# Performance work log

Hardware: AMD Instinct MI355X
Metric: run time of the kernel (lower is better)

## Reference

```python
import jax, jax.numpy as jnp
import numpy as np
from collections import deque

N, IN_DIM, H, B, L = 512, 64, 128, 256, 2
SOURCE = 105
E_UND = 2048


def _build_graph_and_masks():
    rng = np.random.default_rng(0)
    s = rng.integers(0, N, E_UND)
    d = rng.integers(0, N, E_UND)
    edge_index = np.stack([np.concatenate([s, d]), np.concatenate([d, s])]).astype(np.int32)
    # BFS depths from source (undirected)
    adj = [[] for _ in range(N)]
    for a, b in zip(edge_index[0], edge_index[1]):
        adj[int(a)].append(int(b))
    depths = np.full(N, np.inf)
    depths[SOURCE] = 0.0
    q = deque([SOURCE]); seen = {SOURCE}
    while q:
        u = q.popleft()
        for v in adj[u]:
            if v not in seen:
                seen.add(v); depths[v] = depths[u] + 1.0; q.append(v)
    finite = np.isfinite(depths)
    maxd = depths[finite].max() if finite.any() else 0.0
    depths[~finite] = maxd + 1.0
    adj_mask = np.zeros((N, N), np.float32)
    adj_mask[edge_index[0], edge_index[1]] = 1.0
    adj_mask[edge_index[1], edge_index[0]] = 1.0
    np.fill_diagonal(adj_mask, 1.0)
    direction_mask = (depths[None, :] <= depths[:, None]).astype(np.float32)
    # admittance_matrix is None -> uniform init, then masked
    initial_causal = (np.ones((N, N), np.float32) / N) * adj_mask * direction_mask
    return edge_index, adj_mask, direction_mask, initial_causal


def setup_inputs() -> dict:
    key = jax.random.key(0)
    ks = jax.random.split(key, 16)
    edge_index, adj_mask, direction_mask, initial_causal = _build_graph_and_masks()
    w = lambda k, shp: jax.random.normal(k, shp, jnp.float32) * 0.02
    return {
        'x': jax.random.normal(ks[0], (B, N, IN_DIM), jnp.float32),
        'edge_index': jnp.asarray(edge_index),
        'adj_mask': jnp.asarray(adj_mask),
        'direction_mask': jnp.asarray(direction_mask),
        'causal_logits': jnp.asarray(initial_causal),  # nn.Parameter init
        'W_in': w(ks[1], (IN_DIM, H)), 'b_in': jnp.zeros((H,), jnp.float32),
        'Wq': w(ks[2], (H, H)), 'bq': jnp.zeros((H,), jnp.float32),
        'Wk': w(ks[3], (H, H)), 'bk': jnp.zeros((H,), jnp.float32),
        'Wv': w(ks[4], (H, H)), 'bv': jnp.zeros((H,), jnp.float32),
        'gcn_W': w(ks[5], (L, H, H)), 'gcn_b': jnp.zeros((L, H), jnp.float32),
        'W_fuse': w(ks[6], (2 * H, H)), 'b_fuse': jnp.zeros((H,), jnp.float32),
        'ln_g': jnp.ones((H,), jnp.float32), 'ln_b': jnp.zeros((H,), jnp.float32),
    }


def reference(x, edge_index, adj_mask, direction_mask, causal_logits,
              W_in, b_in, Wq, bq, Wk, bk, Wv, bv,
              gcn_W, gcn_b, W_fuse, b_fuse, ln_g, ln_b):
    n = adj_mask.shape[0]
    h = jax.nn.relu(x @ W_in + b_in)                               # (B,N,H)

    # causal matrix: softmax over learned logits, physically masked, renormalized
    C = jax.nn.softmax(causal_logits, axis=-1) * adj_mask * direction_mask
    C = C / jnp.clip(C.sum(-1, keepdims=True), 1e-8)

    # masked causal attention
    Q = h @ Wq + bq; K = h @ Wk + bk; V = h @ Wv + bv
    scale = jnp.asarray(h.shape[-1] ** 0.5, h.dtype)
    attn = jax.nn.softmax(jnp.einsum('bnh,bmh->bnm', Q, K) / scale, axis=-1)
    attn = attn * C[None]
    attn = attn / (attn.sum(-1, keepdims=True) + 1e-8)
    h_causal = jnp.einsum('bnm,bmh->bnh', attn, V)

    # GCNConv stack (self-loops + symmetric norm; dropout is identity in eval)
    src = jnp.concatenate([edge_index[0], jnp.arange(n, dtype=edge_index.dtype)])
    dst = jnp.concatenate([edge_index[1], jnp.arange(n, dtype=edge_index.dtype)])
    deg = jnp.zeros((n,), h.dtype).at[dst].add(1.0)
    dinv = deg ** -0.5                                              # deg>=1 (self loops)
    norm = (dinv[src] * dinv[dst])[None, :, None]                   # (1,E+N,1)
    h_g = h
    for l in range(gcn_W.shape[0]):
        hW = h_g @ gcn_W[l]                                         # (B,N,H)
        msg = hW[:, src, :] * norm                                  # (B,E+N,H)
        h_g = jnp.zeros_like(hW).at[:, dst, :].add(msg) + gcn_b[l]
        h_g = jax.nn.relu(h_g)

    h_comb = jnp.concatenate([h_causal, h_g], axis=-1) @ W_fuse + b_fuse
    mu = h_comb.mean(-1, keepdims=True)
    var = ((h_comb - mu) ** 2).mean(-1, keepdims=True)
    out = (h_comb - mu) / jnp.sqrt(var + 1e-5) * ln_g + ln_b
    return out, C
```

## Files before the change

### kernel.cpp

```cpp
#include <hip/hip_runtime.h>
#include <hip/hip_bf16.h>
#include <math.h>

#define NN 512
#define HH 128
#define INDIM 64
#define BB 256
#define NE 4096
#define MROWS (BB*NN)
#define OUT0 (BB*NN*HH)

typedef __attribute__((ext_vector_type(8))) short short8v;
typedef __attribute__((ext_vector_type(4))) float float4v;

__device__ __forceinline__ unsigned short f2bf(float f) {
  unsigned u = __float_as_uint(f);
  unsigned r = (u + 0x7fffu + ((u >> 16) & 1u)) >> 16;
  return (unsigned short)r;
}
__device__ __forceinline__ float bf2f(unsigned short b) {
  return __uint_as_float(((unsigned)b) << 16);
}

__global__ __launch_bounds__(256) void k_causalC(
    const float* __restrict__ logits, const float* __restrict__ adj,
    const float* __restrict__ dir, float* __restrict__ Cout)
{
  const int row = blockIdx.x;
  const int t = threadIdx.x;
  __shared__ float red[256];
  const float* lrow = logits + (size_t)row * NN;
  float v0 = lrow[t], v1 = lrow[t + 256];
  float mx = fmaxf(v0, v1);
  red[t] = mx; __syncthreads();
  for (int s = 128; s > 0; s >>= 1) { if (t < s) red[t] = fmaxf(red[t], red[t + s]); __syncthreads(); }
  mx = red[0]; __syncthreads();
  float e0 = __expf(v0 - mx), e1 = __expf(v1 - mx);
  red[t] = e0 + e1; __syncthreads();
  for (int s = 128; s > 0; s >>= 1) { if (t < s) red[t] += red[t + s]; __syncthreads(); }
  float sumE = red[0]; __syncthreads();
  float m0 = adj[(size_t)row * NN + t] * dir[(size_t)row * NN + t];
  float m1 = adj[(size_t)row * NN + t + 256] * dir[(size_t)row * NN + t + 256];
  float me0 = e0 * m0, me1 = e1 * m1;
  red[t] = me0 + me1; __syncthreads();
  for (int s = 128; s > 0; s >>= 1) { if (t < s) red[t] += red[t + s]; __syncthreads(); }
  float sumME = red[0];
  float sm = sumME / sumE;
  float denom = fmaxf(sm, 1e-8f) * sumE;
  Cout[(size_t)row * NN + t]       = me0 / denom;
  Cout[(size_t)row * NN + t + 256] = me1 / denom;
}

__global__ __launch_bounds__(512) void k_csr(const int* __restrict__ ei,
                                             int* __restrict__ rp,
                                             int* __restrict__ ci,
                                             float* __restrict__ cw)
{
  __shared__ int scnt[512];
  __shared__ float sdinv[512];
  __shared__ int sval[512];
  __shared__ int scur[512];
  const int t = threadIdx.x;
  const int* src = ei;
  const int* dst = ei + NE;
  scnt[t] = 0;
  __syncthreads();
  for (int e = t; e < NE; e += 512) atomicAdd(&scnt[dst[e]], 1);
  __syncthreads();
  const int deg = scnt[t] + 1;
  sdinv[t] = rsqrtf((float)deg);
  sval[t] = deg;
  __syncthreads();
  for (int off = 1; off < 512; off <<= 1) {
    int add = (t >= off) ? sval[t - off] : 0;
    __syncthreads();
    sval[t] += add;
    __syncthreads();
  }
  const int excl = sval[t] - deg;
  rp[t] = excl;
  if (t == 511) rp[512] = excl + deg;
  ci[excl] = t;
  cw[excl] = sdinv[t] * sdinv[t];
  scur[t] = excl + 1;
  __syncthreads();
  for (int e = t; e < NE; e += 512) {
    int s = src[e], d = dst[e];
    int p = atomicAdd(&scur[d], 1);
    ci[p] = s;
    cw[p] = sdinv[s] * sdinv[d];
  }
}

__global__ __launch_bounds__(512) void k_ccsr(const int* __restrict__ ei,
                                              const float* __restrict__ Cmat,
                                              int* __restrict__ rp,
                                              int* __restrict__ ci,
                                              float* __restrict__ cw)
{
  __shared__ unsigned bm[512 * 16];
  __shared__ int cnt[512];
  __shared__ int sval[512];
  __shared__ int cur[512];
  const int t = threadIdx.x;
  const int* src = ei;
  const int* dst = ei + NE;
  for (int i = t; i < 512 * 16; i += 512) bm[i] = 0u;
  __syncthreads();
  bm[t * 16 + (t >> 5)] |= (1u << (t & 31));
  cnt[t] = 1;
  __syncthreads();
  for (int e = t; e < NE; e += 512) {
    int r = src[e], c = dst[e];
    if (Cmat[(size_t)r * NN + c] > 0.f) {
      unsigned bit = 1u << (c & 31);
      unsigned old = atomicOr(&bm[r * 16 + (c >> 5)], bit);
      if (!(old & bit)) atomicAdd(&cnt[r], 1);
    }
  }
  __syncthreads();
  const int myc = cnt[t];
  sval[t] = myc;
  __syncthreads();
  for (int off = 1; off < 512; off <<= 1) {
    int add = (t >= off) ? sval[t - off] : 0;
    __syncthreads();
    sval[t] += add;
    __syncthreads();
  }
  const int excl = sval[t] - myc;
  rp[t] = excl;
  if (t == 511) rp[512] = excl + myc;
  ci[excl] = t;
  cw[excl] = Cmat[(size_t)t * NN + t];
  cur[t] = excl + 1;
  bm[t * 16 + (t >> 5)] &= ~(1u << (t & 31));
  __syncthreads();
  for (int e = t; e < NE; e += 512) {
    int r = src[e], c = dst[e];
    if (Cmat[(size_t)r * NN + c] > 0.f) {
      unsigned bit = 1u << (c & 31);
      unsigned old = atomicAnd(&bm[r * 16 + (c >> 5)], ~bit);
      if (old & bit) {
        int p = atomicAdd(&cur[r], 1);
        ci[p] = c;
        cw[p] = Cmat[(size_t)r * NN + c];
      }
    }
  }
}

__device__ __forceinline__ void gcn_body(
    int bid, const unsigned short* __restrict__ hW,
    const int* __restrict__ rp, const int* __restrict__ ci,
    const float* __restrict__ cw, const float* __restrict__ bias,
    unsigned short* __restrict__ out, int OS, int OC0)
{
  const int i5 = bid >> 3;
  const int ng = i5 & 31;
  const int b = (bid & 7) * 32 + (i5 >> 5);
  const int t = threadIdx.x;
  const int node = ng * 16 + (t >> 4);
  const int f0 = (t & 15) * 8;

  float bcol[8];
  #pragma unroll
  for (int k = 0; k < 8; k++) bcol[k] = bias[f0 + k];

  const unsigned short* base = hW + (size_t)b * 512 * 128;
  const int beg = rp[node], end = rp[node + 1];
  float acc[8] = {0.f, 0.f, 0.f, 0.f, 0.f, 0.f, 0.f, 0.f};
  for (int j = beg; j < end; j++) {
    int s = ci[j];
    float w = cw[j];
    short8v v = *(const short8v*)&base[(size_t)s * 128 + f0];
    #pragma unroll
    for (int k = 0; k < 8; k++) acc[k] += w * bf2f((unsigned short)v[k]);
  }
  short8v o;
  #pragma unroll
  for (int k = 0; k < 8; k++) {
    float v = fmaxf(acc[k] + bcol[k], 0.f);
    o[k] = (short)f2bf(v);
  }
  *(short8v*)&out[((size_t)(b * 512 + node)) * OS + OC0 + f0] = o;
}

__global__ __launch_bounds__(256) void k_gcn(
    const unsigned short* __restrict__ hW,
    const int* __restrict__ rp, const int* __restrict__ ci,
    const float* __restrict__ cw, const float* __restrict__ bias,
    unsigned short* __restrict__ out, int OS, int OC0)
{
  gcn_body(blockIdx.x, hW, rp, ci, cw, bias, out, OS, OC0);
}

__device__ __forceinline__ void sattn_body(
    int bid, const unsigned short* __restrict__ Qbf,
    const unsigned short* __restrict__ Kbf, const unsigned short* __restrict__ Vbf,
    const int* __restrict__ rp, const int* __restrict__ ci,
    const float* __restrict__ cw, unsigned short* __restrict__ Ocb)
{
  const int i5 = bid >> 3;
  const int ng = i5 & 31;
  const int b = (bid & 7) * 32 + (i5 >> 5);
  const int t = threadIdx.x;
  const int node = ng * 16 + (t >> 4);
  const int f0 = (t & 15) * 8;
  const float scale = 0.088388347648318447f;

  const size_t rowq = ((size_t)(b * 512 + node)) * 128 + f0;
  short8v qv = *(const short8v*)&Qbf[rowq];
  float qf[8];
  #pragma unroll
  for (int k = 0; k < 8; k++) qf[k] = bf2f((unsigned short)qv[k]);

  const unsigned short* Kb = Kbf + (size_t)b * 512 * 128;
  const unsigned short* Vb = Vbf + (size_t)b * 512 * 128;
  const int beg = rp[node], end = rp[node + 1];
  float acc[8] = {0.f, 0.f, 0.f, 0.f, 0.f, 0.f, 0.f, 0.f};
  float sw = 0.f;
  int j = beg;
  float w0 = cw[j];
  int m = ci[j];
  short8v kv = *(const short8v*)&Kb[(size_t)m * 128 + f0];
  short8v vv = *(const short8v*)&Vb[(size_t)m * 128 + f0];
  for (; j < end; ) {
    const int jn = (j + 1 < end) ? j + 1 : j;
    const float w02 = cw[jn];
    const int m2 = ci[jn];
    short8v kv2 = *(const short8v*)&Kb[(size_t)m2 * 128 + f0];
    short8v vv2 = *(const short8v*)&Vb[(size_t)m2 * 128 + f0];
    float part = 0.f;
    #pragma unroll
    for (int k = 0; k < 8; k++) part += qf[k] * bf2f((unsigned short)kv[k]);
    part += __shfl_xor(part, 1);
    part += __shfl_xor(part, 2);
    part += __shfl_xor(part, 4);
    part += __shfl_xor(part, 8);
    float w = __expf(part * scale) * w0;
    sw += w;
    #pragma unroll
    for (int k = 0; k < 8; k++) acc[k] += w * bf2f((unsigned short)vv[k]);
    j++;
    w0 = w02; kv = kv2; vv = vv2;
  }
  float inv = 1.0f / sw;
  short8v o;
  #pragma unroll
  for (int k = 0; k < 8; k++) o[k] = (short)f2bf(acc[k] * inv);
  *(short8v*)&Ocb[((size_t)(b * 512 + node)) * 256 + f0] = o;
}

__global__ __launch_bounds__(256) void k_gs(
    const unsigned short* __restrict__ hW,
    const int* __restrict__ grp, const int* __restrict__ gci,
    const float* __restrict__ gcw, const float* __restrict__ gbias,
    const unsigned short* __restrict__ Qbf, const unsigned short* __restrict__ Kbf,
    const unsigned short* __restrict__ Vbf,
    const int* __restrict__ arp, const int* __restrict__ aci,
    const float* __restrict__ acw,
    unsigned short* __restrict__ Dout)
{
  if (blockIdx.x < 8192)
    gcn_body(blockIdx.x, hW, grp, gci, gcw, gbias, Dout, 256, 128);
  else
    sattn_body(blockIdx.x - 8192, Qbf, Kbf, Vbf, arp, aci, acw, Dout);
}

__global__ __launch_bounds__(256) void k_wt(
    const float* s0, const float* s1, const float* s2, const float* s3,
    const float* s4, const float* s5, const float* s6,
    unsigned short* d0, unsigned short* d1, unsigned short* d2, unsigned short* d3,
    unsigned short* d4, unsigned short* d5, unsigned short* d6)
{
  const float* srcs[7] = {s0, s1, s2, s3, s4, s5, s6};
  unsigned short* dsts[7] = {d0, d1, d2, d3, d4, d5, d6};
  const int Ks[7] = {64, 128, 128, 128, 128, 128, 256};
  const int j = blockIdx.x >> 3;
  const int nc = blockIdx.x & 7;
  const float* s = srcs[j];
  unsigned short* d = dsts[j];
  const int K = Ks[j];
  const int STRW = K + 8;
  const int n0 = nc * 16;
  __shared__ short tile[16 * 264];
  const int t = threadIdx.x;
  for (int i = t; i < K * 16; i += 256) {
    int k = i >> 4, nn = i & 15;
    tile[nn * STRW + k] = (short)f2bf(s[k * 128 + n0 + nn]);
  }
  __syncthreads();
  for (int i = t; i < K * 2; i += 256) {
    int nn = (i * 8) / K;
    int k  = (i * 8) % K;
    *(short8v*)&d[(size_t)(n0 + nn) * K + k] =
        *(const short8v*)&tile[nn * STRW + k];
  }
}

#define GNT 4
template<int KD, bool RELU, bool BATCHW, int OMODE, bool AF32>
__global__ __launch_bounds__(256) void k_bgemm(
    const void* __restrict__ Ap, const unsigned short* __restrict__ Wt,
    const float* __restrict__ bias, void* __restrict__ Out, int OS,
    const float* __restrict__ lng, const float* __restrict__ lnb)
{
  constexpr int KCH = (KD < 128) ? KD : 128;
  constexpr int STR = KCH + 8;
  constexpr bool WONCE = (KD <= 128);
  constexpr int ASH = (64 * STR > 8192) ? 64 * STR : 8192;
  constexpr int TRIPS = KCH / 32;
  __shared__ short lds[ASH + 128 * STR];
  short* As = lds;
  short* Ws = lds + ASH;
  const unsigned short* Abf = (const unsigned short*)Ap;
  const float* Af = (const float*)Ap;
  const int t = threadIdx.x;
  const int wave = t >> 6, lane = t & 63;
  const int l15 = lane & 15, quad = lane >> 4;

  short8v ap[TRIPS];
  float4 fa[TRIPS], fb[TRIPS];

  auto LOADC = [&](int rb, int kc) {
    #pragma unroll
    for (int j = 0; j < TRIPS; j++) {
      int i = t + j * 256;
      int r = i / (KCH / 8), seg = i % (KCH / 8);
      if (AF32) {
        const float* sp = &Af[(size_t)(rb + r) * KD + kc + seg * 8];
        fa[j] = *(const float4*)sp;
        fb[j] = *(const float4*)(sp + 4);
      } else {
        int arow = BATCHW ? ((rb & 511) + r) : (rb + r);
        ap[j] = *(const short8v*)&Abf[(size_t)arow * KD + kc + seg * 8];
      }
    }
  };
  auto STOREC = [&]() {
    #pragma unroll
    for (int j = 0; j < TRIPS; j++) {
      int i = t + j * 256;
      int r = i / (KCH / 8), seg = i % (KCH / 8);
      if (AF32) {
        short8v pk;
        pk[0] = (short)f2bf(fa[j].x); pk[1] = (short)f2bf(fa[j].y);
        pk[2] = (short)f2bf(fa[j].z); pk[3] = (short)f2bf(fa[j].w);
        pk[4] = (short)f2bf(fb[j].x); pk[5] = (short)f2bf(fb[j].y);
        pk[6] = (short)f2bf(fb[j].z); pk[7] = (short)f2bf(fb[j].w);
        *(short8v*)&As[r * STR + seg * 8] = pk;
      } else {
        *(short8v*)&As[r * STR + seg * 8] = ap[j];
      }
    }
  };

  float bcol[8];
  #pragma unroll
  for (int nt = 0; nt < 8; nt++) bcol[nt] = bias ? bias[nt * 16 + l15] : 0.f;
  float gcol[8], bbcol[8];
  if (OMODE == 2) {
    #pragma unroll
    for (int nt = 0; nt < 8; nt++) { gcol[nt] = lng[nt * 16 + l15]; bbcol[nt] = lnb[nt * 16 + l15]; }
  }

  for (int g = blockIdx.x; g < (MROWS / 64) / GNT; g += gridDim.x) {
    if (WONCE) {
      const int b0 = (g * GNT * 64) >> 9;
      const unsigned short* Wb = BATCHW ? (Wt + (size_t)b0 * 128 * KD) : Wt;
      for (int i = t; i < 128 * (KCH / 8); i += 256) {
        int n = i / (KCH / 8), seg = i % (KCH / 8);
        *(short8v*)&Ws[n * STR + seg * 8] =
            *(const short8v*)&Wb[(size_t)n * KD + seg * 8];
      }
    }
    LOADC(g * GNT * 64, 0);
    for (int tt = 0; tt < GNT; tt++) {
      const int tile = g * GNT + tt;
      const int rowbase = tile * 64;
      const int b = rowbase >> 9;
      float4v acc[8];
      #pragma unroll
      for (int nt = 0; nt < 8; nt++) acc[nt] = (float4v){0.f, 0.f, 0.f, 0.f};

      for (int kc = 0; kc < KD; kc += KCH) {
        __syncthreads();
        STOREC();
        if (!WONCE) {
          const unsigned short* Wb = BATCHW ? (Wt + (size_t)b * 128 * KD) : Wt;
          for (int i = t; i < 128 * (KCH / 8); i += 256) {
            int n = i / (KCH / 8), seg = i % (KCH / 8);
            *(short8v*)&Ws[n * STR + seg * 8] =
                *(const short8v*)&Wb[(size_t)n * KD + kc + seg * 8];
          }
        }
        __syncthreads();
        {
          int nkc = kc + KCH, ntt = tt;
          if (nkc >= KD) { nkc = 0; ntt = tt + 1; }
          if (ntt < GNT) LOADC((g * GNT + ntt) * 64, nkc);
        }
        #pragma unroll
        for (int k32 = 0; k32 < KCH / 32; k32++) {
          short8v af = *(const short8v*)&As[(wave * 16 + l15) * STR + k32 * 32 + quad * 8];
          #pragma unroll
          for (int nt = 0; nt < 8; nt++) {
            short8v wf = *(const short8v*)&Ws[(nt * 16 + l15) * STR + k32 * 32 + quad * 8];
            acc[nt] = __builtin_amdgcn_mfma_f32_16x16x32_bf16(af, wf, acc[nt], 0, 0, 0);
          }
        }
      }

      __syncthreads();
      if (OMODE == 0) {
        short* rep = As + wave * 2048;
        #pragma unroll
        for (int nt = 0; nt < 8; nt++)
          #pragma unroll
          for (int r = 0; r < 4; r++) {
            float v = acc[nt][r] + bcol[nt];
            if (RELU) v = fmaxf(v, 0.f);
            rep[(quad * 4 + r) * 128 + nt * 16 + l15] = (short)f2bf(v);
          }
        __syncthreads();
        unsigned short* Ob = (unsigned short*)Out;
        #pragma unroll
        for (int p = 0; p < 4; p++) {
          int row16 = (lane >> 4) + p * 4, seg = lane & 15;
          short8v vv = *(const short8v*)&rep[row16 * 128 + seg * 8];
          *(short8v*)&Ob[(size_t)(rowbase + wave * 16 + row16) * OS + seg * 8] = vv;
        }
      } else if (OMODE == 1) {
        short* rep = As + wave * 2048;
        #pragma unroll
        for (int nt = 0; nt < 8; nt++)
          #pragma unroll
          for (int r = 0; r < 4; r++) {
            float v = acc[nt][r] + bcol[nt];
            if (RELU) v = fmaxf(v, 0.f);
            rep[(nt * 16 + l15) * 16 + quad * 4 + r] = (short)f2bf(v);
          }
        __syncthreads();
        unsigned short* Ob = (unsigned short*)Out;
        int node0 = (rowbase & 511) + wave * 16;
        #pragma unroll
        for (int p = 0; p < 4; p++) {
          int idx = p * 64 + lane, c = idx >> 1, half = idx & 1;
          short8v vv = *(const short8v*)&rep[c * 16 + half * 8];
          *(short8v*)&Ob[((size_t)(b * 128 + c)) * 512 + node0 + half * 8] = vv;
        }
      } else {
        float* repw = (float*)lds + wave * 2048;
        float vv[8][4];
        float s[4] = {0, 0, 0, 0}, ss[4] = {0, 0, 0, 0};
        #pragma unroll
        for (int nt = 0; nt < 8; nt++)
          #pragma unroll
          for (int r = 0; r < 4; r++) {
            float v = acc[nt][r] + bcol[nt];
            vv[nt][r] = v;
            s[r] += v; ss[r] += v * v;
          }
        #pragma unroll
        for (int r = 0; r < 4; r++) {
          s[r] += __shfl_xor(s[r], 1);  s[r] += __shfl_xor(s[r], 2);
          s[r] += __shfl_xor(s[r], 4);  s[r] += __shfl_xor(s[r], 8);
          ss[r] += __shfl_xor(ss[r], 1); ss[r] += __shfl_xor(ss[r], 2);
          ss[r] += __shfl_xor(ss[r], 4); ss[r] += __shfl_xor(ss[r], 8);
        }
        #pragma unroll
        for (int r = 0; r < 4; r++) {
          float mu = s[r] * (1.0f / 128.0f);
          float var = ss[r] * (1.0f / 128.0f) - mu * mu;
          float inv = rsqrtf(var + 1e-5f);
          #pragma unroll
          for (int nt = 0; nt < 8; nt++)
            repw[(quad * 4 + r) * 128 + nt * 16 + l15] =
                (vv[nt][r] - mu) * inv * gcol[nt] + bbcol[nt];
        }
        __syncthreads();
        float* Of = (float*)Out;
        #pragma unroll
        for (int p = 0; p < 8; p++) {
          int row16 = (lane >> 5) + p * 2, seg = lane & 31;
          float4 o = *(const float4*)&repw[row16 * 128 + seg * 4];
          *(float4*)&Of[(size_t)(rowbase + wave * 16 + row16) * 128 + seg * 4] = o;
        }
      }
    }
  }
}

__global__ __launch_bounds__(256) void k_qkv4(
    const unsigned short* __restrict__ Abf,
    const unsigned short* __restrict__ W0, const unsigned short* __restrict__ W1,
    const unsigned short* __restrict__ W2, const unsigned short* __restrict__ W3,
    const float* __restrict__ b1, const float* __restrict__ b2,
    const float* __restrict__ b3,
    unsigned short* __restrict__ O0, unsigned short* __restrict__ O1,
    unsigned short* __restrict__ O2, unsigned short* __restrict__ O3)
{
  constexpr int STR = 136;
  __shared__ short lds[8704 + 128 * STR];
  short* As = lds;
  short* Ws = lds + 8704;
  const int t = threadIdx.x;
  const int wave = t >> 6, lane = t & 63;
  const int l15 = lane & 15, quad = lane >> 4;

  const unsigned short* Wsrc[4] = {W0, W1, W2, W3};
  const float* Bsrc[4] = {nullptr, b1, b2, b3};
  unsigned short* Osrc[4] = {O0, O1, O2, O3};

  short8v ap[4];
  auto LOADC = [&](int rb) {
    #pragma unroll
    for (int j = 0; j < 4; j++) {
      int i = t + j * 256;
      int r = i >> 4, seg = i & 15;
      ap[j] = *(const short8v*)&Abf[(size_t)(rb + r) * 128 + seg * 8];
    }
  };

  for (int g = blockIdx.x; g < (MROWS / 64) / GNT; g += gridDim.x) {
    #pragma unroll
    for (int s = 0; s < 4; s++) {
      for (int i = t; i < 128 * 16; i += 256) {
        int n = i >> 4, seg = i & 15;
        *(short8v*)&Ws[n * STR + seg * 8] =
            *(const short8v*)&Wsrc[s][(size_t)n * 128 + seg * 8];
      }
      float bcol[8];
      #pragma unroll
      for (int nt = 0; nt < 8; nt++) bcol[nt] = Bsrc[s] ? Bsrc[s][nt * 16 + l15] : 0.f;
      if (s == 0) LOADC(g * GNT * 64);

      for (int tt = 0; tt < GNT; tt++) {
        const int rowbase = (g * GNT + tt) * 64;
        float4v acc[8];
        #pragma unroll
        for (int nt = 0; nt < 8; nt++) acc[nt] = (float4v){0.f, 0.f, 0.f, 0.f};

        __syncthreads();
        #pragma unroll
        for (int j = 0; j < 4; j++) {
          int i = t + j * 256;
          int r = i >> 4, seg = i & 15;
          *(short8v*)&As[r * STR + seg * 8] = ap[j];
        }
        __syncthreads();

        {
          int ntt = tt + 1;
          if (ntt < GNT) LOADC((g * GNT + ntt) * 64);
          else if (s < 3) LOADC(g * GNT * 64);
        }

        #pragma unroll
        for (int k32 = 0; k32 < 4; k32++) {
          short8v af = *(const short8v*)&As[(wave * 16 + l15) * STR + k32 * 32 + quad * 8];
          #pragma unroll
          for (int nt = 0; nt < 8; nt++) {
            short8v wf = *(const short8v*)&Ws[(nt * 16 + l15) * STR + k32 * 32 + quad * 8];
            acc[nt] = __builtin_amdgcn_mfma_f32_16x16x32_bf16(af, wf, acc[nt], 0, 0, 0);
          }
        }
        __syncthreads();

        unsigned short* Ob = Osrc[s];
        short* rep = As + wave * 2048;
        #pragma unroll
        for (int nt = 0; nt < 8; nt++)
          #pragma unroll
          for (int r = 0; r < 4; r++) {
            float v = acc[nt][r] + bcol[nt];
            rep[(quad * 4 + r) * 128 + nt * 16 + l15] = (short)f2bf(v);
          }
        __syncthreads();
        #pragma unroll
        for (int p = 0; p < 4; p++) {
          int row16 = (lane >> 4) + p * 4, seg = lane & 15;
          short8v vv = *(const short8v*)&rep[row16 * 128 + seg * 8];
          *(short8v*)&Ob[(size_t)(rowbase + wave * 16 + row16) * 128 + seg * 8] = vv;
        }
      }
    }
  }
}

extern "C" void kernel_launch(void* const* d_in, const int* in_sizes, int n_in,
                              void* d_out, int out_size, void* d_ws, size_t ws_size,
                              hipStream_t stream)
{
  const float* x     = (const float*)d_in[0];
  const int*   ei    = (const int*)d_in[1];
  const float* adj   = (const float*)d_in[2];
  const float* dmask = (const float*)d_in[3];
  const float* clog  = (const float*)d_in[4];
  const float* W_in  = (const float*)d_in[5];
  const float* b_in  = (const float*)d_in[6];
  const float* Wq    = (const float*)d_in[7];
  const float* bq    = (const float*)d_in[8];
  const float* Wk    = (const float*)d_in[9];
  const float* bk    = (const float*)d_in[10];
  const float* Wv    = (const float*)d_in[11];
  const float* bv    = (const float*)d_in[12];
  const float* gcnW  = (const float*)d_in[13];
  const float* gcnB  = (const float*)d_in[14];
  const float* Wf    = (const float*)d_in[15];
  const float* bf    = (const float*)d_in[16];
  const float* lng   = (const float*)d_in[17];
  const float* lnb   = (const float*)d_in[18];

  float* outp = (float*)d_out;
  float* Cmat = outp + OUT0;

  char* W = (char*)d_ws;
  const size_t SLOT = (size_t)MROWS * 128 * 2;
  unsigned short* A0 = (unsigned short*)(W);
  unsigned short* B0 = (unsigned short*)(W + SLOT);
  unsigned short* C0 = (unsigned short*)(W + 2 * SLOT);
  unsigned short* D0 = (unsigned short*)(W + 3 * SLOT);
  char* AUX = W + 5 * SLOT;
  int*   csr_rp = (int*)AUX;
  int*   csr_ci = csr_rp + 640;
  float* csr_cw = (float*)(csr_ci + 4608);
  int*   crp    = (int*)(AUX + 131072);
  int*   cci    = crp + 640;
  float* ccw    = (float*)(cci + 8192);
  unsigned short* WB    = (unsigned short*)(AUX + 512 * 512 * 4) + 512 * 512 * 2;
  unsigned short* W_int = WB;
  unsigned short* Wqt   = WB + 8192;
  unsigned short* Wkt   = Wqt + 16384;
  unsigned short* Wvt   = Wkt + 16384;
  unsigned short* G0t   = Wvt + 16384;
  unsigned short* G1t   = G0t + 16384;
  unsigned short* Wft   = G1t + 16384;

  unsigned short* Vbf = (unsigned short*)outp;
  unsigned short* E0  = Vbf + (size_t)MROWS * 128;

  k_causalC<<<512, 256, 0, stream>>>(clog, adj, dmask, Cmat);
  k_csr<<<1, 512, 0, stream>>>(ei, csr_rp, csr_ci, csr_cw);
  k_ccsr<<<1, 512, 0, stream>>>(ei, Cmat, crp, cci, ccw);
  k_wt<<<56, 256, 0, stream>>>(W_in, Wq, Wk, Wv, gcnW, gcnW + HH * HH, Wf,
                               W_int, Wqt, Wkt, Wvt, G0t, G1t, Wft);

  k_bgemm<64, true, false, 0, true><<<512, 256, 0, stream>>>(
      x, W_int, b_in, B0, 128, nullptr, nullptr);
  k_qkv4<<<512, 256, 0, stream>>>(
      B0, G0t, Wqt, Wkt, Wvt, bq, bk, bv, A0, C0, E0, Vbf);
  k_gcn<<<8192, 256, 0, stream>>>(A0, csr_rp, csr_ci, csr_cw, gcnB, B0, 128, 0);
  k_bgemm<128, false, false, 0, false><<<512, 256, 0, stream>>>(
      B0, G1t, nullptr, A0, 128, nullptr, nullptr);
  k_gs<<<16384, 256, 0, stream>>>(
      A0, csr_rp, csr_ci, csr_cw, gcnB + HH,
      C0, E0, Vbf, crp, cci, ccw, D0);
  k_bgemm<256, false, false, 2, false><<<512, 256, 0, stream>>>(
      D0, Wft, bf, outp, 128, lng, lnb);
}
```

Before: 392.8 us.

## Replace second GCN weight GEMM with persistent per-wave MFMA kernel

Adds a persistent GEMM kernel for the 128x128 GCN layer-1 weight multiply. Each block loads the transposed weight into LDS once, and each wave walks 16-row tiles with register double-buffered A fragments. Each wave stages its output through a private LDS slice so it can write coalesced 16-byte stores. This cuts the per-block weight reloads and launch granularity of the generic batched GEMM, at the cost of extra LDS use and lower occupancy per block.

```diff
diff --git a/kernel.cpp b/kernel.cpp
--- a/kernel.cpp
+++ b/kernel.cpp
@@ -299,6 +299,79 @@
   }
 }
 
+template<bool RELU>
+__global__ __launch_bounds__(256) void k_wgemm(
+    const unsigned short* __restrict__ Abf,
+    const unsigned short* __restrict__ Wt,
+    const float* __restrict__ bias,
+    unsigned short* __restrict__ Out)
+{
+  constexpr int STR = 136;
+  __shared__ short Ws[128 * STR];
+  __shared__ short rep[4 * 2048];
+  const int t = threadIdx.x;
+  const int wave = t >> 6, lane = t & 63;
+  const int l15 = lane & 15, quad = lane >> 4;
+  short* rw = rep + wave * 2048;
+
+  for (int i = t; i < 128 * 16; i += 256) {
+    int n = i >> 4, seg = i & 15;
+    *(short8v*)&Ws[n * STR + seg * 8] =
+        *(const short8v*)&Wt[(size_t)n * 128 + seg * 8];
+  }
+  float bcol[8];
+  #pragma unroll
+  for (int nt = 0; nt < 8; nt++) bcol[nt] = bias ? bias[nt * 16 + l15] : 0.f;
+  __syncthreads();
+
+  const int nwaves = gridDim.x * 4;
+  int tile = blockIdx.x * 4 + wave;
+  short8v af[4], afn[4];
+  if (tile < MROWS / 16) {
+    #pragma unroll
+    for (int dc = 0; dc < 4; dc++)
+      af[dc] = *(const short8v*)&Abf[((size_t)(tile * 16 + l15)) * 128 + dc * 32 + quad * 8];
+  }
+  while (tile < MROWS / 16) {
+    const int ntile = tile + nwaves;
+    if (ntile < MROWS / 16) {
+      #pragma unroll
+      for (int dc = 0; dc < 4; dc++)
+        afn[dc] = *(const short8v*)&Abf[((size_t)(ntile * 16 + l15)) * 128 + dc * 32 + quad * 8];
+    }
+    float4v acc[8];
+    #pragma unroll
+    for (int nt = 0; nt < 8; nt++) acc[nt] = (float4v){0.f, 0.f, 0.f, 0.f};
+    #pragma unroll
+    for (int k32 = 0; k32 < 4; k32++) {
+      #pragma unroll
+      for (int nt = 0; nt < 8; nt++) {
+        short8v wf = *(const short8v*)&Ws[(nt * 16 + l15) * STR + k32 * 32 + quad * 8];
+        acc[nt] = __builtin_amdgcn_mfma_f32_16x16x32_bf16(af[k32], wf, acc[nt], 0, 0, 0);
+      }
+    }
+    #pragma unroll
+    for (int nt = 0; nt < 8; nt++)
+      #pragma unroll
+      for (int r = 0; r < 4; r++) {
+        float v = acc[nt][r] + bcol[nt];
+        if (RELU) v = fmaxf(v, 0.f);
+        rw[(quad * 4 + r) * 128 + nt * 16 + l15] = (short)f2bf(v);
+      }
+    asm volatile("s_waitcnt lgkmcnt(0)" ::: "memory");
+    __builtin_amdgcn_sched_barrier(0);
+    #pragma unroll
+    for (int p = 0; p < 4; p++) {
+      int row16 = (lane >> 4) + p * 4, seg = lane & 15;
+      short8v vv = *(const short8v*)&rw[row16 * 128 + seg * 8];
+      *(short8v*)&Out[((size_t)(tile * 16 + row16)) * 128 + seg * 8] = vv;
+    }
+    tile = ntile;
+    #pragma unroll
+    for (int dc = 0; dc < 4; dc++) af[dc] = afn[dc];
+  }
+}
+
 #define GNT 4
 template<int KD, bool RELU, bool BATCHW, int OMODE, bool AF32>
 __global__ __launch_bounds__(256) void k_bgemm(
@@ -652,8 +725,7 @@
   k_qkv4<<<512, 256, 0, stream>>>(
       B0, G0t, Wqt, Wkt, Wvt, bq, bk, bv, A0, C0, E0, Vbf);
   k_gcn<<<8192, 256, 0, stream>>>(A0, csr_rp, csr_ci, csr_cw, gcnB, B0, 128, 0);
-  k_bgemm<128, false, false, 0, false><<<512, 256, 0, stream>>>(
-      B0, G1t, nullptr, A0, 128, nullptr, nullptr);
+  k_wgemm<false><<<768, 256, 0, stream>>>(B0, G1t, nullptr, A0);
   k_gs<<<16384, 256, 0, stream>>>(
       A0, csr_rp, csr_ci, csr_cw, gcnB + HH,
       C0, E0, Vbf, crp, cci, ccw, D0);
```

After: 393.7 us. Within noise of the previous version (+0.2%).
